# Kernel tuning notes

Measured on AMD Instinct MI355X. Metric: run time of the kernel, lower is better.

Reference implementation:

```python
import jax, jax.numpy as jnp
import numpy as np

STRIDE, PAD, DIL, K = 1, 1, 1, 3  # from init_kwargs; kernel hardcoded 3x3 in module


def setup_inputs() -> dict:
    key = jax.random.key(0)
    k1, k2, k3, k4, k5 = jax.random.split(key, 5)
    B, C, H, W, O = 8, 128, 64, 64, 128
    inp = jax.random.normal(k1, (B, C, H, W), jnp.float32)
    # offsets in pixels; small magnitudes are typical of learned DCN offsets
    offset = jax.random.normal(k2, (B, 2 * K * K, H, W), jnp.float32)
    mask = jax.random.uniform(k3, (B, K * K, H, W), dtype=jnp.float32)  # modulation in [0,1)
    weight = jax.random.normal(k4, (O, C, K, K), jnp.float32) * 0.05
    bias = jax.random.normal(k5, (O,), jnp.float32) * 0.05
    return {"input": inp, "offset": offset, "mask": mask, "weight": weight, "bias": bias}


def reference(input, offset, mask, weight, bias):
    B, C, H, W = input.shape
    O = weight.shape[0]
    Ho = (H + 2 * PAD - DIL * (K - 1) - 1) // STRIDE + 1
    Wo = (W + 2 * PAD - DIL * (K - 1) - 1) // STRIDE + 1

    # torchvision layout: offset[:, 2k] = dy, offset[:, 2k+1] = dx for kernel tap k
    off = offset.reshape(B, K * K, 2, Ho, Wo)
    off_y, off_x = off[:, :, 0], off[:, :, 1]  # [B, 9, Ho, Wo]

    kh, kw = jnp.meshgrid(jnp.arange(K), jnp.arange(K), indexing="ij")
    kh, kw = kh.reshape(-1), kw.reshape(-1)  # [9]

    # absolute (fractional) sampling positions per output pixel and kernel tap
    py = (jnp.arange(Ho) * STRIDE - PAD)[None, None, :, None] + (kh * DIL)[None, :, None, None] + off_y
    px = (jnp.arange(Wo) * STRIDE - PAD)[None, None, None, :] + (kw * DIL)[None, :, None, None] + off_x

    y0 = jnp.floor(py)
    x0 = jnp.floor(px)
    wy1 = py - y0  # fractional parts
    wx1 = px - x0

    inp_bhwc = jnp.transpose(input, (0, 2, 3, 1))  # [B, H, W, C] for clean gather
    b_idx = jnp.arange(B)[:, None, None, None]

    def corner(yc, xc, w):
        # zero-padded bilinear: out-of-bounds corners contribute 0
        valid = (yc >= 0) & (yc < H) & (xc >= 0) & (xc < W)
        ycl = jnp.clip(yc, 0, H - 1).astype(jnp.int32)
        xcl = jnp.clip(xc, 0, W - 1).astype(jnp.int32)
        v = inp_bhwc[b_idx, ycl, xcl]  # [B, 9, Ho, Wo, C]
        return v * (w * valid)[..., None]

    sampled = (corner(y0, x0, (1 - wy1) * (1 - wx1))
               + corner(y0, x0 + 1, (1 - wy1) * wx1)
               + corner(y0 + 1, x0, wy1 * (1 - wx1))
               + corner(y0 + 1, x0 + 1, wy1 * wx1))  # [B, 9, Ho, Wo, C]

    sampled = sampled * mask[..., None]  # DCNv2 modulation

    out = jnp.einsum("bkhwc,ock->bohw", sampled, weight.reshape(O, C, K * K))
    return out + bias[None, :, None, None]
```

## Files before the change

### kernel.cpp

```cpp
#include <hip/hip_runtime.h>

#define BB 8
#define CC 128
#define HH 64
#define WW 64
#define OO 128
#define KT 9
#define HWs (HH * WW)

typedef __attribute__((ext_vector_type(8))) _Float16 half8;
typedef __attribute__((ext_vector_type(8))) short short8;
typedef __attribute__((ext_vector_type(8))) unsigned short ushort8;
typedef __attribute__((ext_vector_type(4))) float f32x4;

__device__ inline unsigned short f2bf(float f) {
    union { float f; unsigned int u; } x; x.f = f;
    unsigned int u = x.u;
    unsigned int r = u + 0x7fff + ((u >> 16) & 1);
    return (unsigned short)(r >> 16);
}

__device__ __forceinline__ void gload_lds16(const void* g, void* l) {
    __builtin_amdgcn_global_load_lds(
        (__attribute__((address_space(1))) void*)g,
        (__attribute__((address_space(3))) void*)l, 16, 0, 0);
}

__global__ __launch_bounds__(256) void prep_input(
    const float* __restrict__ in, _Float16* __restrict__ out) {
    __shared__ float t[CC][33];
    int b = blockIdx.y;
    int s0 = blockIdx.x * 32;
    int s = threadIdx.x & 31;
    int c0 = threadIdx.x >> 5;
    const float* ip = in + (size_t)b * CC * HWs;
#pragma unroll
    for (int c = 0; c < CC; c += 8)
        t[c + c0][s] = ip[(size_t)(c + c0) * HWs + s0 + s];
    __syncthreads();
    int ws = threadIdx.x >> 3;
    int cg = (threadIdx.x & 7) * 16;
    _Float16 v[16];
#pragma unroll
    for (int i = 0; i < 16; ++i) v[i] = (_Float16)t[cg + i][ws];
    _Float16* op = out + ((size_t)(b * HWs) + s0 + ws) * CC + cg;
    *(half8*)op = *(half8*)&v[0];
    *(half8*)(op + 8) = *(half8*)&v[8];
}

__global__ __launch_bounds__(256) void prep_weight(
    const float* __restrict__ w, unsigned short* __restrict__ wbf) {
    int i = blockIdx.x * 256 + threadIdx.x;
    if (i >= KT * OO * CC) return;
    int k = i / (OO * CC);
    int r = i % (OO * CC);
    int o = r >> 7, c = r & 127;
    unsigned byte = (unsigned)(o * 256 + ((2 * c) ^ ((o & 15) << 4)));
    *(unsigned short*)((char*)wbf + (size_t)k * 32768 + byte) =
        f2bf(w[o * (CC * KT) + c * KT + k]);
}

__global__ __launch_bounds__(256, 2) void deform_sample(
    const _Float16* __restrict__ inh, const float* __restrict__ offset,
    const float* __restrict__ mask, unsigned short* __restrict__ As,
    int b0, int lnb) {
    int nb = 1 << lnb;
    int hw = blockIdx.x;
    int xcd = hw & 7;
    int j = hw >> 3;
    int bl = xcd & (nb - 1);
    int task = (xcd >> lnb) * (144 << lnb) + j;
    int tap = task >> 7;
    int blk = task & 127;
    int tid = threadIdx.x;
    int px = blk * 32 + (tid >> 3);
    int cg = (tid & 7) * 16;
    int ho = px >> 6, wo = px & 63;
    int b = b0 + bl;

    const _Float16* base = inh + (size_t)b * HWs * CC;
    float oy = offset[(size_t)(b * 18 + 2 * tap) * HWs + ho * WW + wo];
    float ox = offset[(size_t)(b * 18 + 2 * tap + 1) * HWs + ho * WW + wo];
    float mm = mask[(size_t)(b * 9 + tap) * HWs + ho * WW + wo];

    int kh = tap / 3, kw = tap % 3;
    float py = (float)(ho - 1 + kh) + oy;
    float pxf = (float)(wo - 1 + kw) + ox;
    float fy = floorf(py), fx = floorf(pxf);
    float wy1 = py - fy, wx1 = pxf - fx;
    float wy0 = 1.f - wy1, wx0 = 1.f - wx1;
    int y0 = (int)fy, x0 = (int)fx;
    int y1 = y0 + 1, x1 = x0 + 1;
    bool vy0 = (y0 >= 0) & (y0 < HH);
    bool vy1 = (y1 >= 0) & (y1 < HH);
    bool vx0 = (x0 >= 0) & (x0 < WW);
    bool vx1 = (x1 >= 0) & (x1 < WW);
    float w00 = (vy0 & vx0) ? wy0 * wx0 * mm : 0.f;
    float w01 = (vy0 & vx1) ? wy0 * wx1 * mm : 0.f;
    float w10 = (vy1 & vx0) ? wy1 * wx0 * mm : 0.f;
    float w11 = (vy1 & vx1) ? wy1 * wx1 * mm : 0.f;
    int y0c = min(max(y0, 0), HH - 1), y1c = min(max(y1, 0), HH - 1);
    int x0c = min(max(x0, 0), WW - 1), x1c = min(max(x1, 0), WW - 1);
    const _Float16* p00 = base + (size_t)(y0c * WW + x0c) * CC + cg;
    const _Float16* p01 = base + (size_t)(y0c * WW + x1c) * CC + cg;
    const _Float16* p10 = base + (size_t)(y1c * WW + x0c) * CC + cg;
    const _Float16* p11 = base + (size_t)(y1c * WW + x1c) * CC + cg;
    half8 g00a = *(const half8*)p00, g00b = *(const half8*)(p00 + 8);
    half8 g01a = *(const half8*)p01, g01b = *(const half8*)(p01 + 8);
    half8 g10a = *(const half8*)p10, g10b = *(const half8*)(p10 + 8);
    half8 g11a = *(const half8*)p11, g11b = *(const half8*)(p11 + 8);

    ushort8 o0, o1;
#pragma unroll
    for (int q = 0; q < 8; ++q) {
        float s = w00 * (float)g00a[q] + w01 * (float)g01a[q] +
                  w10 * (float)g10a[q] + w11 * (float)g11a[q];
        o0[q] = f2bf(s);
    }
#pragma unroll
    for (int q = 0; q < 8; ++q) {
        float s = w00 * (float)g00b[q] + w01 * (float)g01b[q] +
                  w10 * (float)g10b[q] + w11 * (float)g11b[q];
        o1[q] = f2bf(s);
    }
    char* rowp = (char*)As + ((size_t)bl * 4096 + px) * 2304 + tap * 256;
    unsigned sw = (unsigned)((px & 15) << 4);
    *(ushort8*)(rowp + ((2 * cg) ^ sw)) = o0;
    *(ushort8*)(rowp + ((2 * cg + 16) ^ sw)) = o1;
}

__global__ __launch_bounds__(256, 2) void deform_gemm(
    const unsigned short* __restrict__ As, const unsigned short* __restrict__ wbf,
    const float* __restrict__ bias, float* __restrict__ out, int b0) {
    __shared__ unsigned short Al[64 * 128];
    __shared__ unsigned short Bl[OO * CC];

    int bpx = blockIdx.x * 64;
    int tid = threadIdx.x;
    int wv = tid >> 6, l = tid & 63;
    int lr = l & 15, lg = l >> 4;

    const char* bwsrc = (const char*)wbf + (size_t)wv * 8192 + (size_t)l * 16;
    char* bldst = (char*)Bl + wv * 8192;

    f32x4 acc[8] = {};

    for (int k = 0; k < KT; ++k) {
        __syncthreads();
        {
            const char* s = bwsrc + (size_t)k * 32768;
#pragma unroll
            for (int j2 = 0; j2 < 8; ++j2)
                gload_lds16(s + j2 * 1024, bldst + j2 * 1024);
        }
        {
#pragma unroll
            for (int j2 = 0; j2 < 4; ++j2) {
                int row = wv * 16 + j2 * 4 + lg;
                const char* s = (const char*)As +
                    (size_t)(bpx + row) * 2304 + (size_t)k * 256 + lr * 16;
                gload_lds16(s, (char*)Al + (wv * 16 + j2 * 4) * 256);
            }
        }
        __syncthreads();

#pragma unroll
        for (int c32 = 0; c32 < 4; ++c32) {
            int arow = wv * 16 + lr;
            unsigned ab = (unsigned)(arow * 256 + ((c32 * 64 + lg * 16) ^ (lr << 4)));
            short8 af = *(const short8*)((const char*)Al + ab);
#pragma unroll
            for (int n = 0; n < 8; ++n) {
                int o = n * 16 + lr;
                unsigned bb = (unsigned)(o * 256 + ((c32 * 64 + lg * 16) ^ (lr << 4)));
                short8 bf = *(const short8*)((const char*)Bl + bb);
                acc[n] = __builtin_amdgcn_mfma_f32_16x16x32_bf16(
                    af, bf, acc[n], 0, 0, 0);
            }
        }
    }

    int sp0 = bpx + wv * 16 + lg * 4;
    int b = b0 + (sp0 >> 12);
    int sp = sp0 & 4095;
    int ho = sp >> 6;
    int wo0 = sp & 63;
#pragma unroll
    for (int n = 0; n < 8; ++n) {
        int o = n * 16 + lr;
        float bs = bias[o];
        float4 v;
        v.x = acc[n][0] + bs;
        v.y = acc[n][1] + bs;
        v.z = acc[n][2] + bs;
        v.w = acc[n][3] + bs;
        *(float4*)(out + (size_t)(b * OO + o) * HWs + ho * WW + wo0) = v;
    }
}

extern "C" void kernel_launch(void* const* d_in, const int* in_sizes, int n_in,
                              void* d_out, int out_size, void* d_ws, size_t ws_size,
                              hipStream_t stream) {
    const float* inp    = (const float*)d_in[0];
    const float* offset = (const float*)d_in[1];
    const float* mask   = (const float*)d_in[2];
    const float* weight = (const float*)d_in[3];
    const float* bias   = (const float*)d_in[4];
    float* out = (float*)d_out;

    const size_t inh_b = (size_t)BB * HWs * CC * sizeof(_Float16);
    const size_t wbf_b = (size_t)KT * OO * CC * sizeof(unsigned short);
    _Float16* inh = (_Float16*)d_ws;
    unsigned short* wbf = (unsigned short*)((char*)d_ws + inh_b);
    unsigned short* As = (unsigned short*)((char*)d_ws + inh_b + wbf_b);

    size_t avail = (ws_size > inh_b + wbf_b) ? ws_size - inh_b - wbf_b : 0;
    int lnb = 3;
    while (lnb > 0 && ((size_t)(1 << lnb)) * 4096u * 2304u > avail) --lnb;
    int nb = 1 << lnb;

    prep_input<<<dim3(128, 8), 256, 0, stream>>>(inp, inh);
    prep_weight<<<dim3((KT * OO * CC + 255) / 256), 256, 0, stream>>>(weight, wbf);
    for (int b0 = 0; b0 < BB; b0 += nb) {
        deform_sample<<<dim3(nb * 1152), 256, 0, stream>>>(
            inh, offset, mask, As, b0, lnb);
        deform_gemm<<<dim3(nb * 64), 256, 0, stream>>>(As, wbf, bias, out, b0);
    }
}
```

Baseline: 53.85 us.

## Double-buffer weight tiles and load A fragments directly into registers in GEMM

New measurement: 57.05 us. 5.9% more time.

```diff
diff --git a/kernel.cpp b/kernel.cpp
--- a/kernel.cpp
+++ b/kernel.cpp
@@ -60,7 +60,7 @@
         f2bf(w[o * (CC * KT) + c * KT + k]);
 }
 
-__global__ __launch_bounds__(256, 2) void deform_sample(
+__global__ __launch_bounds__(256, 4) void deform_sample(
     const _Float16* __restrict__ inh, const float* __restrict__ offset,
     const float* __restrict__ mask, unsigned short* __restrict__ As,
     int b0, int lnb) {
@@ -124,16 +124,14 @@
         o1[q] = f2bf(s);
     }
     char* rowp = (char*)As + ((size_t)bl * 4096 + px) * 2304 + tap * 256;
-    unsigned sw = (unsigned)((px & 15) << 4);
-    *(ushort8*)(rowp + ((2 * cg) ^ sw)) = o0;
-    *(ushort8*)(rowp + ((2 * cg + 16) ^ sw)) = o1;
+    *(ushort8*)(rowp + 2 * cg) = o0;
+    *(ushort8*)(rowp + 2 * cg + 16) = o1;
 }
 
 __global__ __launch_bounds__(256, 2) void deform_gemm(
     const unsigned short* __restrict__ As, const unsigned short* __restrict__ wbf,
     const float* __restrict__ bias, float* __restrict__ out, int b0) {
-    __shared__ unsigned short Al[64 * 128];
-    __shared__ unsigned short Bl[OO * CC];
+    __shared__ unsigned short Bl[2][OO * CC];
 
     int bpx = blockIdx.x * 64;
     int tid = threadIdx.x;
@@ -141,43 +139,48 @@
     int lr = l & 15, lg = l >> 4;
 
     const char* bwsrc = (const char*)wbf + (size_t)wv * 8192 + (size_t)l * 16;
-    char* bldst = (char*)Bl + wv * 8192;
+    const char* aptr = (const char*)As + (size_t)(bpx + wv * 16 + lr) * 2304 +
+                       (size_t)lg * 16;
 
     f32x4 acc[8] = {};
-
+    int4 areg[2][4];
+
+#pragma unroll
+    for (int j2 = 0; j2 < 8; ++j2)
+        gload_lds16(bwsrc + j2 * 1024, (char*)Bl[0] + wv * 8192 + j2 * 1024);
+#pragma unroll
+    for (int c32 = 0; c32 < 4; ++c32)
+        areg[0][c32] = *(const int4*)(aptr + c32 * 64);
+    __syncthreads();
+
+#pragma unroll
     for (int k = 0; k < KT; ++k) {
-        __syncthreads();
-        {
-            const char* s = bwsrc + (size_t)k * 32768;
+        if (k < KT - 1) {
+            const char* s = bwsrc + (size_t)(k + 1) * 32768;
+            char* d = (char*)Bl[(k + 1) & 1] + wv * 8192;
 #pragma unroll
             for (int j2 = 0; j2 < 8; ++j2)
-                gload_lds16(s + j2 * 1024, bldst + j2 * 1024);
+                gload_lds16(s + j2 * 1024, d + j2 * 1024);
+#pragma unroll
+            for (int c32 = 0; c32 < 4; ++c32)
+                areg[(k + 1) & 1][c32] =
+                    *(const int4*)(aptr + (k + 1) * 256 + c32 * 64);
         }
-        {
-#pragma unroll
-            for (int j2 = 0; j2 < 4; ++j2) {
-                int row = wv * 16 + j2 * 4 + lg;
-                const char* s = (const char*)As +
-                    (size_t)(bpx + row) * 2304 + (size_t)k * 256 + lr * 16;
-                gload_lds16(s, (char*)Al + (wv * 16 + j2 * 4) * 256);
-            }
-        }
-        __syncthreads();
 
 #pragma unroll
         for (int c32 = 0; c32 < 4; ++c32) {
-            int arow = wv * 16 + lr;
-            unsigned ab = (unsigned)(arow * 256 + ((c32 * 64 + lg * 16) ^ (lr << 4)));
-            short8 af = *(const short8*)((const char*)Al + ab);
+            short8 af = *(const short8*)&areg[k & 1][c32];
 #pragma unroll
             for (int n = 0; n < 8; ++n) {
                 int o = n * 16 + lr;
                 unsigned bb = (unsigned)(o * 256 + ((c32 * 64 + lg * 16) ^ (lr << 4)));
-                short8 bf = *(const short8*)((const char*)Bl + bb);
+                short8 bf = *(const short8*)((const char*)Bl[k & 1] + bb);
                 acc[n] = __builtin_amdgcn_mfma_f32_16x16x32_bf16(
                     af, bf, acc[n], 0, 0, 0);
             }
         }
+
+        if (k < KT - 1) __syncthreads();
     }
 
     int sp0 = bpx + wv * 16 + lg * 4;
```
